# Kernel tuning notes

Measured on AMD Instinct MI355X. Metric: run time of the kernel, lower is better.

Reference implementation:

```python
import jax, jax.numpy as jnp
import numpy as np

B, T, E = 2, 2048, 2048
H, HKV, DH = 16, 8, 128
G = H // HKV
WINDOW = 512
ROPE_THETA = 10000.0
EPS = 1e-6


def _rms_norm(x, w):
    # Gemma3RMSNorm: fp32 rms_norm with weight = 1 + w
    xf = x.astype(jnp.float32)
    y = xf * jax.lax.rsqrt(jnp.mean(xf * xf, axis=-1, keepdims=True) + EPS)
    return (y * (1.0 + w.astype(jnp.float32))).astype(x.dtype)


def _rotate_half(x):
    x1, x2 = x[..., : DH // 2], x[..., DH // 2 :]
    return jnp.concatenate((-x2, x1), axis=-1)


def setup_inputs() -> dict:
    key = jax.random.key(0)
    ks = jax.random.split(key, 5)
    s = 0.02
    return {
        "x": jax.random.normal(ks[0], (B, T, E), jnp.float32),
        "wq": jax.random.normal(ks[1], (H * DH, E), jnp.float32) * s,
        "wk": jax.random.normal(ks[2], (HKV * DH, E), jnp.float32) * s,
        "wv": jax.random.normal(ks[3], (HKV * DH, E), jnp.float32) * s,
        "wo": jax.random.normal(ks[4], (E, H * DH), jnp.float32) * s,
        "q_norm_w": jnp.zeros((DH,), jnp.float32),
        "k_norm_w": jnp.zeros((DH,), jnp.float32),
    }


def reference(x, wq, wk, wv, wo, q_norm_w, k_norm_w):
    # projections: [B,T,H,DH] -> [B,H,T,DH]
    q = (x @ wq.T).reshape(B, T, H, DH).transpose(0, 2, 1, 3)
    k = (x @ wk.T).reshape(B, T, HKV, DH).transpose(0, 2, 1, 3)
    v = (x @ wv.T).reshape(B, T, HKV, DH).transpose(0, 2, 1, 3)

    # QK-RMSNorm over head_dim
    q = _rms_norm(q, q_norm_w)
    k = _rms_norm(k, k_norm_w)

    # RoPE (prefill: positions 0..T-1)
    pos = jnp.arange(T, dtype=jnp.float32)
    inv_freq = 1.0 / (ROPE_THETA ** (jnp.arange(0, DH, 2, dtype=jnp.float32) / DH))
    freqs = pos[:, None] * inv_freq[None, :]          # [T, DH//2]
    emb = jnp.concatenate((freqs, freqs), axis=-1)    # [T, DH]
    cos = jnp.cos(emb)[None, None, :, :]
    sin = jnp.sin(emb)[None, None, :, :]
    q = q * cos + _rotate_half(q) * sin
    k = k * cos + _rotate_half(k) * sin

    # GQA attention with causal + sliding-window mask, fp32 scores
    q = q * (DH ** -0.5)
    qg = q.reshape(B, HKV, G, T, DH)
    att = jnp.einsum("bhgtd,bhkd->bhgtk", qg.astype(jnp.float32), k.astype(jnp.float32))

    dist = jnp.arange(T)[:, None] - jnp.arange(T)[None, :]   # [T, T]
    mask = (dist >= 0) & (dist <= WINDOW)
    att = jnp.where(mask[None, None, None, :, :], att, jnp.finfo(jnp.float32).min)
    att = jax.nn.softmax(att, axis=-1).astype(q.dtype)

    ctx = jnp.einsum("bhgtk,bhkd->bhgtd", att, v)
    out = ctx.reshape(B, H, T, DH).transpose(0, 2, 1, 3).reshape(B, T, H * DH)
    return out @ wo.T
```

## Files before the change

### kernel.cpp

```cpp
#include <hip/hip_runtime.h>
#include <hip/hip_bf16.h>
#include <stdint.h>

#define B_ 2
#define T_ 2048
#define E_ 2048
#define H_ 16
#define HKV_ 8
#define DH_ 128
#define WINDOW_ 512

typedef unsigned short ush;
typedef float f32x4 __attribute__((ext_vector_type(4)));
typedef __bf16 bf16x8 __attribute__((ext_vector_type(8)));
typedef uint32_t u32x4 __attribute__((ext_vector_type(4)));

static __device__ __forceinline__ ush f2bf(float f) {
    uint32_t u = __float_as_uint(f);
    uint32_t r = (u + 0x7fffu + ((u >> 16) & 1u)) >> 16;
    return (ush)r;
}
static __device__ __forceinline__ float bf2f(ush h) {
    return __uint_as_float(((uint32_t)h) << 16);
}

__global__ __launch_bounds__(256) void cast_kernel(const float* __restrict__ in,
                                                   ush* __restrict__ out, int n4) {
    int i = blockIdx.x * blockDim.x + threadIdx.x;
    if (i >= n4) return;
    float4 f = reinterpret_cast<const float4*>(in)[i];
    ushort4 o;
    o.x = f2bf(f.x); o.y = f2bf(f.y); o.z = f2bf(f.z); o.w = f2bf(f.w);
    reinterpret_cast<ushort4*>(out)[i] = o;
}

template <int MODE>
__global__ __launch_bounds__(512, 2) void gemm_bt2(
    const ush* __restrict__ A, const ush* __restrict__ Bm,
    float* __restrict__ Cf, ush* __restrict__ q, ush* __restrict__ k, ush* __restrict__ vT,
    int M, int N, int K)
{
    __shared__ ush As[3][128 * 64];
    __shared__ ush Bs[3][256 * 64];
    const int tid = threadIdx.x;
    const int lane = tid & 63;
    const int wid = tid >> 6;
    const int wr = wid >> 2, wc = wid & 3;
    const int g = lane >> 4, t = lane & 15;
    const int gm0 = blockIdx.x * 128, gn0 = blockIdx.y * 256;

    f32x4 acc[4][4] = {};

    auto stageA2 = [&](int kt, int m3) {
#pragma unroll
        for (int i = 0; i < 2; ++i) {
            const int C = i * 512 + tid;
            const int r = C >> 3, c = C & 7;
            const ush* src = A + (size_t)(gm0 + r) * K + (kt << 6) + ((c ^ (r & 7)) << 3);
            __builtin_amdgcn_global_load_lds(
                (const __attribute__((address_space(1))) void*)src,
                (__attribute__((address_space(3))) void*)(&As[m3][C << 3]), 16, 0, 0);
        }
    };
    auto stageB = [&](int kt, int m3, int i0, int i1) {
        for (int i = i0; i < i1; ++i) {
            const int C = i * 512 + tid;
            const int r = C >> 3, c = C & 7;
            const ush* src = Bm + (size_t)(gn0 + r) * K + (kt << 6) + ((c ^ (r & 7)) << 3);
            __builtin_amdgcn_global_load_lds(
                (const __attribute__((address_space(1))) void*)src,
                (__attribute__((address_space(3))) void*)(&Bs[m3][C << 3]), 16, 0, 0);
        }
    };

    const int nt = K >> 6;

    stageA2(0, 0); stageB(0, 0, 0, 4);
    stageA2(1, 1); stageB(1, 1, 0, 4);
    asm volatile("s_waitcnt vmcnt(6)" ::: "memory");
    __builtin_amdgcn_s_barrier();
    __builtin_amdgcn_sched_barrier(0);

    int m3 = 0;
    for (int kt = 0; kt < nt; ++kt) {
        const int st3 = (m3 + 2 >= 3) ? m3 - 1 : m3 + 2;
        bf16x8 af[4][2], bfr[2][2];

#pragma unroll
        for (int mf = 0; mf < 4; ++mf)
#pragma unroll
            for (int ks = 0; ks < 2; ++ks) {
                const int row = wr * 64 + mf * 16 + t;
                af[mf][ks] = *reinterpret_cast<const bf16x8*>(
                    &As[m3][row * 64 + ((((ks << 2) + g) ^ (t & 7)) << 3)]);
            }
#pragma unroll
        for (int n2 = 0; n2 < 2; ++n2)
#pragma unroll
            for (int ks = 0; ks < 2; ++ks) {
                const int row = wc * 64 + n2 * 16 + t;
                bfr[n2][ks] = *reinterpret_cast<const bf16x8*>(
                    &Bs[m3][row * 64 + ((((ks << 2) + g) ^ (t & 7)) << 3)]);
            }
        if (kt + 2 < nt) { stageA2(kt + 2, st3); stageB(kt + 2, st3, 0, 1); }
        __builtin_amdgcn_s_setprio(1);
#pragma unroll
        for (int mf = 0; mf < 4; ++mf)
#pragma unroll
            for (int n2 = 0; n2 < 2; ++n2)
#pragma unroll
                for (int ks = 0; ks < 2; ++ks)
                    acc[mf][n2] = __builtin_amdgcn_mfma_f32_16x16x32_bf16(
                        af[mf][ks], bfr[n2][ks], acc[mf][n2], 0, 0, 0);
        __builtin_amdgcn_s_setprio(0);
        __builtin_amdgcn_s_barrier();
        __builtin_amdgcn_sched_barrier(0);

#pragma unroll
        for (int n2 = 0; n2 < 2; ++n2)
#pragma unroll
            for (int ks = 0; ks < 2; ++ks) {
                const int row = wc * 64 + (2 + n2) * 16 + t;
                bfr[n2][ks] = *reinterpret_cast<const bf16x8*>(
                    &Bs[m3][row * 64 + ((((ks << 2) + g) ^ (t & 7)) << 3)]);
            }
        if (kt + 2 < nt) stageB(kt + 2, st3, 1, 4);
        __builtin_amdgcn_s_setprio(1);
#pragma unroll
        for (int mf = 0; mf < 4; ++mf)
#pragma unroll
            for (int n2 = 0; n2 < 2; ++n2)
#pragma unroll
                for (int ks = 0; ks < 2; ++ks)
                    acc[mf][2 + n2] = __builtin_amdgcn_mfma_f32_16x16x32_bf16(
                        af[mf][ks], bfr[n2][ks], acc[mf][2 + n2], 0, 0, 0);
        __builtin_amdgcn_s_setprio(0);
        if (kt + 1 < nt) {
            if (kt + 2 < nt) asm volatile("s_waitcnt vmcnt(6)" ::: "memory");
            else             asm volatile("s_waitcnt vmcnt(0)" ::: "memory");
        }
        __builtin_amdgcn_s_barrier();
        __builtin_amdgcn_sched_barrier(0);

        m3 = (m3 + 1 >= 3) ? 0 : m3 + 1;
    }

    const int rsub = (lane >> 4) << 2;
    const int csub = lane & 15;
#pragma unroll
    for (int mf = 0; mf < 4; ++mf) {
        const int row0 = gm0 + wr * 64 + mf * 16 + rsub;
#pragma unroll
        for (int nf = 0; nf < 4; ++nf) {
            const int col = gn0 + wc * 64 + nf * 16 + csub;
#pragma unroll
            for (int r = 0; r < 4; ++r) {
                const int row = row0 + r;
                if (MODE == 1) {
                    Cf[(size_t)row * N + col] = acc[mf][nf][r];
                } else {
                    const int bb = row >> 11, tt = row & (T_ - 1);
                    const ush val = f2bf(acc[mf][nf][r]);
                    if (col < H_ * DH_) {
                        const int hh = col >> 7, d = col & 127;
                        q[((((size_t)bb * H_ + hh) * T_ + tt) << 7) + d] = val;
                    } else if (col < H_ * DH_ + HKV_ * DH_) {
                        const int c2 = col - H_ * DH_;
                        const int hh = c2 >> 7, d = c2 & 127;
                        k[((((size_t)bb * HKV_ + hh) * T_ + tt) << 7) + d] = val;
                    } else {
                        const int c2 = col - H_ * DH_ - HKV_ * DH_;
                        const int hh = c2 >> 7, d = c2 & 127;
                        vT[((size_t)((bb * HKV_ + hh) * DH_ + d) << 11) + tt] = val;
                    }
                }
            }
        }
    }
}

__global__ __launch_bounds__(256) void norm_rope(ush* __restrict__ q, ush* __restrict__ k,
                                                 const float* __restrict__ qw,
                                                 const float* __restrict__ kw)
{
    const int lane = threadIdx.x & 63;
    const int row = blockIdx.x * 4 + (threadIdx.x >> 6);
    const int NQ = B_ * H_ * T_;
    ush* p; const float* w; int t; bool isq = (row < NQ);
    if (isq) { p = q + ((size_t)row << 7); t = row & (T_ - 1); w = qw; }
    else     { int r2 = row - NQ; p = k + ((size_t)r2 << 7); t = r2 & (T_ - 1); w = kw; }

    float x0 = bf2f(p[lane]);
    float x1 = bf2f(p[lane + 64]);
    float ss = x0 * x0 + x1 * x1;
#pragma unroll
    for (int off = 32; off; off >>= 1) ss += __shfl_xor(ss, off);
    const float rms = rsqrtf(ss * (1.0f / 128.0f) + 1e-6f);
    float y0 = x0 * rms * (1.0f + w[lane]);
    float y1 = x1 * rms * (1.0f + w[lane + 64]);

    const float invf = expf(-(float)lane * 0.14391156831212787f);
    const float fr = (float)t * invf;
    const float c = cosf(fr), s = sinf(fr);
    float o0 = y0 * c - y1 * s;
    float o1 = y1 * c + y0 * s;
    if (isq) { o0 *= 0.08838834764831845f; o1 *= 0.08838834764831845f; }
    p[lane] = f2bf(o0);
    p[lane + 64] = f2bf(o1);
}

__global__ __launch_bounds__(256) void attn_mfma(const ush* __restrict__ q,
        const ush* __restrict__ k, const ush* __restrict__ vT, ush* __restrict__ ctx)
{
    __shared__ ush Ks[2][32 * 128];
    __shared__ ush Vs[2][128 * 32];
    const int tid = threadIdx.x;
    const int lane = tid & 63;
    const int w = tid >> 6;
    const int g = lane >> 4;
    const int t = lane & 15;

    int bi = blockIdx.x;
    bi = (bi & 7) * 128 + (bi >> 3);
    const int qtile = bi & 31;
    const int hh = (bi >> 5) & 15;
    const int b = bi >> 9;
    const int qb = qtile * 64;
    const int hkv = hh >> 1;

    const ush* qptr = q + ((((size_t)b * H_ + hh) * T_ + qb) << 7);
    const ush* kbase = k + (((size_t)b * HKV_ + hkv) << 18);
    const ush* vtbase = vT + (((size_t)b * HKV_ + hkv) << 18);

    bf16x8 qf[4];
#pragma unroll
    for (int c = 0; c < 4; ++c)
        qf[c] = *reinterpret_cast<const bf16x8*>(qptr + ((16 * w + t) << 7) + 32 * c + 8 * g);

    const int kstart = (qb >= WINDOW_) ? (qb - WINDOW_) : 0;
    const int nt = (qb + 64 - kstart) >> 5;

    auto stage = [&](int ti, int buf) {
        const int kt0 = kstart + (ti << 5);
#pragma unroll
        for (int i = 0; i < 2; ++i) {
            const int C = w * 128 + i * 64 + lane;
            {
                const int row = C >> 4, ch = C & 15;
                const ush* gk = kbase + ((size_t)(kt0 + row) << 7) + ch * 8;
                __builtin_amdgcn_global_load_lds(
                    (const __attribute__((address_space(1))) void*)gk,
                    (__attribute__((address_space(3))) void*)(&Ks[buf][(w * 128 + i * 64) * 8]),
                    16, 0, 0);
            }
            {
                const int row = C >> 2, ch = C & 3;
                const ush* gv = vtbase + ((size_t)row << 11) + kt0 + ch * 8;
                __builtin_amdgcn_global_load_lds(
                    (const __attribute__((address_space(1))) void*)gv,
                    (__attribute__((address_space(3))) void*)(&Vs[buf][(w * 128 + i * 64) * 8]),
                    16, 0, 0);
            }
        }
    };

    float m = -1e30f, lsum = 0.f;
    f32x4 o[8] = {};

    stage(0, 0);
    __syncthreads();

    for (int ti = 0; ti < nt; ++ti) {
        const int cur = ti & 1;
        if (ti + 1 < nt) stage(ti + 1, cur ^ 1);
        const int kt0 = kstart + (ti << 5);
        const int qw0 = qb + 16 * w;
        const bool active = (kt0 + 31 >= qw0 - WINDOW_) && (kt0 <= qw0 + 15);
        if (active) {
            f32x4 st[2] = {};
#pragma unroll
            for (int s = 0; s < 2; ++s)
#pragma unroll
                for (int c = 0; c < 4; ++c) {
                    bf16x8 kf = *reinterpret_cast<const bf16x8*>(
                        &Ks[cur][(16 * s + t) * 128 + 32 * c + 8 * g]);
                    st[s] = __builtin_amdgcn_mfma_f32_16x16x32_bf16(kf, qf[c], st[s], 0, 0, 0);
                }
            const int tg = qb + 16 * w + t;
            float e[2][4];
            float mymax = -3e38f;
#pragma unroll
            for (int s = 0; s < 2; ++s)
#pragma unroll
                for (int r = 0; r < 4; ++r) {
                    const int key = kt0 + 16 * s + 4 * g + r;
                    const int dist = tg - key;
                    const bool valid = (dist >= 0) && (dist <= WINDOW_);
                    const float sv = valid ? st[s][r] : -3e38f;
                    e[s][r] = sv;
                    mymax = fmaxf(mymax, sv);
                }
            mymax = fmaxf(mymax, __shfl_xor(mymax, 16));
            mymax = fmaxf(mymax, __shfl_xor(mymax, 32));
            const float mn = fmaxf(m, mymax);
            const float sc = __expf(m - mn);
            float esum = 0.f;
#pragma unroll
            for (int s = 0; s < 2; ++s)
#pragma unroll
                for (int r = 0; r < 4; ++r) {
                    const float ev = __expf(e[s][r] - mn);
                    e[s][r] = ev;
                    esum += ev;
                }
            esum += __shfl_xor(esum, 16);
            esum += __shfl_xor(esum, 32);
            lsum = lsum * sc + esum;
            m = mn;
#pragma unroll
            for (int ds = 0; ds < 8; ++ds) {
                o[ds][0] *= sc; o[ds][1] *= sc; o[ds][2] *= sc; o[ds][3] *= sc;
            }
            uint32_t word[2][2];
#pragma unroll
            for (int s = 0; s < 2; ++s)
#pragma unroll
                for (int wd = 0; wd < 2; ++wd)
                    word[s][wd] = (uint32_t)f2bf(e[s][2 * wd])
                                | ((uint32_t)f2bf(e[s][2 * wd + 1]) << 16);
            u32x4 bw;
#pragma unroll
            for (int e2 = 0; e2 < 4; ++e2) {
                const int srcl = 16 * (2 * (g & 1) + (e2 >> 1)) + t;
                const uint32_t v0 = __shfl(word[0][e2 & 1], srcl);
                const uint32_t v1 = __shfl(word[1][e2 & 1], srcl);
                bw[e2] = (g >= 2) ? v1 : v0;
            }
            const bf16x8 pF = __builtin_bit_cast(bf16x8, bw);
#pragma unroll
            for (int ds = 0; ds < 8; ++ds) {
                bf16x8 vtF = *reinterpret_cast<const bf16x8*>(
                    &Vs[cur][(16 * ds + t) * 32 + 8 * g]);
                o[ds] = __builtin_amdgcn_mfma_f32_16x16x32_bf16(vtF, pF, o[ds], 0, 0, 0);
            }
        }
        __syncthreads();
    }

    const float linv = 1.0f / lsum;
    ush* cptr = ctx + (((size_t)b * T_ + qb + 16 * w + t) * (H_ * DH_)) + hh * DH_;
#pragma unroll
    for (int ds = 0; ds < 8; ++ds) {
        ushort4 pk;
        pk.x = f2bf(o[ds][0] * linv);
        pk.y = f2bf(o[ds][1] * linv);
        pk.z = f2bf(o[ds][2] * linv);
        pk.w = f2bf(o[ds][3] * linv);
        *reinterpret_cast<ushort4*>(cptr + 16 * ds + 4 * g) = pk;
    }
}

extern "C" void kernel_launch(void* const* d_in, const int* in_sizes, int n_in,
                              void* d_out, int out_size, void* d_ws, size_t ws_size,
                              hipStream_t stream)
{
    const float* x   = (const float*)d_in[0];
    const float* wq  = (const float*)d_in[1];
    const float* wk  = (const float*)d_in[2];
    const float* wv  = (const float*)d_in[3];
    const float* wo  = (const float*)d_in[4];
    const float* qnw = (const float*)d_in[5];
    const float* knw = (const float*)d_in[6];
    float* out = (float*)d_out;

    ush* ws    = (ush*)d_ws;
    ush* xbf   = ws;
    ush* wqkv  = xbf  + 8388608;
    ush* wobf  = wqkv + 8388608;
    ush* qraw  = wobf + 4194304;
    ush* kraw  = qraw + 8388608;
    ush* vTb   = kraw + 4194304;
    ush* ctx   = vTb  + 4194304;

    cast_kernel<<<8192, 256, 0, stream>>>(x,  xbf, 2097152);
    cast_kernel<<<4096, 256, 0, stream>>>(wq, wqkv, 1048576);
    cast_kernel<<<2048, 256, 0, stream>>>(wk, wqkv + 4194304, 524288);
    cast_kernel<<<2048, 256, 0, stream>>>(wv, wqkv + 6291456, 524288);
    cast_kernel<<<4096, 256, 0, stream>>>(wo, wobf, 1048576);

    gemm_bt2<0><<<dim3(32, 16), 512, 0, stream>>>(xbf, wqkv, nullptr, qraw, kraw, vTb,
                                                  4096, 4096, 2048);
    norm_rope<<<(65536 + 32768) / 4, 256, 0, stream>>>(qraw, kraw, qnw, knw);
    attn_mfma<<<1024, 256, 0, stream>>>(qraw, kraw, vTb, ctx);
    gemm_bt2<1><<<dim3(32, 8), 512, 0, stream>>>(ctx, wobf, out, nullptr, nullptr, nullptr,
                                                 4096, 2048, 2048);
    (void)in_sizes; (void)n_in; (void)out_size; (void)ws_size;
}
```

Before: 232.7 us.

## Merge cast launches and restructure GEMM main loop into single-phase k-step

The five fp32-to-bf16 cast launches become one grid-stride kernel that writes the contiguous workspace. In the GEMM, each k-step now loads all four B fragments from LDS, issues all next-tile global-to-LDS loads at once, and runs all 32 MFMAs in one phase. This drops the intermediate barrier and the split B staging. It saves launch overhead and one barrier per k-step, but uses more fragment registers and gives less interleaving of loads with MFMA work.

Measured after the change: 236.8 us. About the same (+1.8%).

```diff
diff --git a/kernel.cpp b/kernel.cpp
--- a/kernel.cpp
+++ b/kernel.cpp
@@ -24,18 +24,27 @@
     return __uint_as_float(((uint32_t)h) << 16);
 }
 
-__global__ __launch_bounds__(256) void cast_kernel(const float* __restrict__ in,
-                                                   ush* __restrict__ out, int n4) {
-    int i = blockIdx.x * blockDim.x + threadIdx.x;
-    if (i >= n4) return;
-    float4 f = reinterpret_cast<const float4*>(in)[i];
-    ushort4 o;
-    o.x = f2bf(f.x); o.y = f2bf(f.y); o.z = f2bf(f.z); o.w = f2bf(f.w);
-    reinterpret_cast<ushort4*>(out)[i] = o;
+__global__ __launch_bounds__(256) void cast_all(const float* __restrict__ x,
+        const float* __restrict__ wq, const float* __restrict__ wk,
+        const float* __restrict__ wv, const float* __restrict__ wo,
+        ush* __restrict__ dst) {
+    const int stride = gridDim.x * blockDim.x;
+    for (int i = blockIdx.x * blockDim.x + threadIdx.x; i < 5242880; i += stride) {
+        const float4* src;
+        if (i < 2097152)      src = (const float4*)x  + i;
+        else if (i < 3145728) src = (const float4*)wq + (i - 2097152);
+        else if (i < 3670016) src = (const float4*)wk + (i - 3145728);
+        else if (i < 4194304) src = (const float4*)wv + (i - 3670016);
+        else                  src = (const float4*)wo + (i - 4194304);
+        const float4 f = *src;
+        ushort4 o;
+        o.x = f2bf(f.x); o.y = f2bf(f.y); o.z = f2bf(f.z); o.w = f2bf(f.w);
+        reinterpret_cast<ushort4*>(dst)[i] = o;
+    }
 }
 
 template <int MODE>
-__global__ __launch_bounds__(512, 2) void gemm_bt2(
+__global__ __launch_bounds__(512, 2) void gemm_bt3(
     const ush* __restrict__ A, const ush* __restrict__ Bm,
     float* __restrict__ Cf, ush* __restrict__ q, ush* __restrict__ k, ush* __restrict__ vT,
     int M, int N, int K)
@@ -62,8 +71,9 @@
                 (__attribute__((address_space(3))) void*)(&As[m3][C << 3]), 16, 0, 0);
         }
     };
-    auto stageB = [&](int kt, int m3, int i0, int i1) {
-        for (int i = i0; i < i1; ++i) {
+    auto stageB4 = [&](int kt, int m3) {
+#pragma unroll
+        for (int i = 0; i < 4; ++i) {
             const int C = i * 512 + tid;
             const int r = C >> 3, c = C & 7;
             const ush* src = Bm + (size_t)(gn0 + r) * K + (kt << 6) + ((c ^ (r & 7)) << 3);
@@ -75,8 +85,8 @@
 
     const int nt = K >> 6;
 
-    stageA2(0, 0); stageB(0, 0, 0, 4);
-    stageA2(1, 1); stageB(1, 1, 0, 4);
+    stageA2(0, 0); stageB4(0, 0);
+    stageA2(1, 1); stageB4(1, 1);
     asm volatile("s_waitcnt vmcnt(6)" ::: "memory");
     __builtin_amdgcn_s_barrier();
     __builtin_amdgcn_sched_barrier(0);
@@ -84,7 +94,7 @@
     int m3 = 0;
     for (int kt = 0; kt < nt; ++kt) {
         const int st3 = (m3 + 2 >= 3) ? m3 - 1 : m3 + 2;
-        bf16x8 af[4][2], bfr[2][2];
+        bf16x8 af[4][2], bfr[4][2];
 
 #pragma unroll
         for (int mf = 0; mf < 4; ++mf)
@@ -95,46 +105,27 @@
                     &As[m3][row * 64 + ((((ks << 2) + g) ^ (t & 7)) << 3)]);
             }
 #pragma unroll
-        for (int n2 = 0; n2 < 2; ++n2)
+        for (int nf = 0; nf < 4; ++nf)
 #pragma unroll
             for (int ks = 0; ks < 2; ++ks) {
-                const int row = wc * 64 + n2 * 16 + t;
-                bfr[n2][ks] = *reinterpret_cast<const bf16x8*>(
+                const int row = wc * 64 + nf * 16 + t;
+                bfr[nf][ks] = *reinterpret_cast<const bf16x8*>(
                     &Bs[m3][row * 64 + ((((ks << 2) + g) ^ (t & 7)) << 3)]);
             }
-        if (kt + 2 < nt) { stageA2(kt + 2, st3); stageB(kt + 2, st3, 0, 1); }
+
+        if (kt + 2 < nt) { stageA2(kt + 2, st3); stageB4(kt + 2, st3); }
+
         __builtin_amdgcn_s_setprio(1);
 #pragma unroll
-        for (int mf = 0; mf < 4; ++mf)
-#pragma unroll
-            for (int n2 = 0; n2 < 2; ++n2)
-#pragma unroll
-                for (int ks = 0; ks < 2; ++ks)
-                    acc[mf][n2] = __builtin_amdgcn_mfma_f32_16x16x32_bf16(
-                        af[mf][ks], bfr[n2][ks], acc[mf][n2], 0, 0, 0);
+        for (int ks = 0; ks < 2; ++ks)
+#pragma unroll
+            for (int mf = 0; mf < 4; ++mf)
+#pragma unroll
+                for (int nf = 0; nf < 4; ++nf)
+                    acc[mf][nf] = __builtin_amdgcn_mfma_f32_16x16x32_bf16(
+                        af[mf][ks], bfr[nf][ks], acc[mf][nf], 0, 0, 0);
         __builtin_amdgcn_s_setprio(0);
-        __builtin_amdgcn_s_barrier();
-        __builtin_amdgcn_sched_barrier(0);
-
-#pragma unroll
-        for (int n2 = 0; n2 < 2; ++n2)
-#pragma unroll
-            for (int ks = 0; ks < 2; ++ks) {
-                const int row = wc * 64 + (2 + n2) * 16 + t;
-                bfr[n2][ks] = *reinterpret_cast<const bf16x8*>(
-                    &Bs[m3][row * 64 + ((((ks << 2) + g) ^ (t & 7)) << 3)]);
-            }
-        if (kt + 2 < nt) stageB(kt + 2, st3, 1, 4);
-        __builtin_amdgcn_s_setprio(1);
-#pragma unroll
-        for (int mf = 0; mf < 4; ++mf)
-#pragma unroll
-            for (int n2 = 0; n2 < 2; ++n2)
-#pragma unroll
-                for (int ks = 0; ks < 2; ++ks)
-                    acc[mf][2 + n2] = __builtin_amdgcn_mfma_f32_16x16x32_bf16(
-                        af[mf][ks], bfr[n2][ks], acc[mf][2 + n2], 0, 0, 0);
-        __builtin_amdgcn_s_setprio(0);
+
         if (kt + 1 < nt) {
             if (kt + 2 < nt) asm volatile("s_waitcnt vmcnt(6)" ::: "memory");
             else             asm volatile("s_waitcnt vmcnt(0)" ::: "memory");
@@ -382,17 +373,13 @@
     ush* vTb   = kraw + 4194304;
     ush* ctx   = vTb  + 4194304;
 
-    cast_kernel<<<8192, 256, 0, stream>>>(x,  xbf, 2097152);
-    cast_kernel<<<4096, 256, 0, stream>>>(wq, wqkv, 1048576);
-    cast_kernel<<<2048, 256, 0, stream>>>(wk, wqkv + 4194304, 524288);
-    cast_kernel<<<2048, 256, 0, stream>>>(wv, wqkv + 6291456, 524288);
-    cast_kernel<<<4096, 256, 0, stream>>>(wo, wobf, 1048576);
-
-    gemm_bt2<0><<<dim3(32, 16), 512, 0, stream>>>(xbf, wqkv, nullptr, qraw, kraw, vTb,
+    cast_all<<<2048, 256, 0, stream>>>(x, wq, wk, wv, wo, ws);
+
+    gemm_bt3<0><<<dim3(32, 16), 512, 0, stream>>>(xbf, wqkv, nullptr, qraw, kraw, vTb,
                                                   4096, 4096, 2048);
     norm_rope<<<(65536 + 32768) / 4, 256, 0, stream>>>(qraw, kraw, qnw, knw);
     attn_mfma<<<1024, 256, 0, stream>>>(qraw, kraw, vTb, ctx);
-    gemm_bt2<1><<<dim3(32, 8), 512, 0, stream>>>(ctx, wobf, out, nullptr, nullptr, nullptr,
+    gemm_bt3<1><<<dim3(32, 8), 512, 0, stream>>>(ctx, wobf, out, nullptr, nullptr, nullptr,
                                                  4096, 2048, 2048);
     (void)in_sizes; (void)n_in; (void)out_size; (void)ws_size;
 }
```
